# Performance work log

Measured on AMD Instinct MI355X. Metric: run time of the kernel, lower is better.

Reference implementation:

```python
import jax, jax.numpy as jnp
import numpy as np

MAX_RANGE = 100.0


def _conv3x3(x, w, b):
    # x: [B,C,H,W], w: [2,C,3,3], b: [2]
    y = jax.lax.conv_general_dilated(
        x, w, window_strides=(1, 1), padding='SAME',
        dimension_numbers=('NCHW', 'OIHW', 'NCHW'))
    return y + b[None, :, None, None]


def setup_inputs() -> dict:
    key = jax.random.key(0)
    k1, k2, k3 = jax.random.split(key, 3)
    B, C, H, W = 4, 64, 64, 64
    x = jax.random.normal(k1, (B, C, H, W), dtype=jnp.float32)
    conv_w = jax.random.normal(k2, (2, C, 3, 3), dtype=jnp.float32) * 0.05
    conv_b = jax.random.normal(k3, (2,), dtype=jnp.float32) * 0.05
    return {'x': x, 'conv_w': conv_w, 'conv_b': conv_b}


def reference(x, conv_w, conv_b):
    # alpha, beta: [B,1,H,W]
    ab = MAX_RANGE * jnp.tanh(_conv3x3(x, conv_w, conv_b))
    alpha, beta = ab[:, 0:1], ab[:, 1:2]

    # Pairwise differences d[b,i,j,h,w] = beta[b]*x[b,i] - x[b,j]  -> [B,C,C,H,W]
    d = beta[:, :, None] * x[:, :, None] - x[:, None, :]
    a = alpha[:, :, None]  # [B,1,1,H,W]

    # softAbs: softmax over the pair {d, -d} weighted by clamped alpha*d logits
    v1 = jnp.clip(d * a, -MAX_RANGE, MAX_RANGE)
    v2 = jnp.clip(-d * a, -MAX_RANGE, MAX_RANGE)
    m = jnp.maximum(v1, v2)
    e1 = jnp.exp(v1 - m)
    e2 = jnp.exp(v2 - m)
    p1 = e1 / (e1 + e2)
    sabs = d * (2.0 * p1 - 1.0)  # d*p1 + (-d)*(1-p1)

    # mean over i (the expand dim) -> [B,C,H,W]
    tmp = jnp.mean(sabs, axis=1)

    # softArgMin over channel dim
    sam = jax.nn.softmax(jnp.clip(-tmp * alpha, -MAX_RANGE, MAX_RANGE), axis=1)

    # soft median, keepdims -> [B,1,H,W]
    return jnp.sum(x * sam, axis=1, keepdims=True)
```

## Files before the change

kernel.cpp:

```cpp
#include <hip/hip_runtime.h>
#include <math.h>

#define MAXR 100.0f

__device__ __forceinline__ float tanh_fast(float s) {
    float as = fabsf(s);
    float e2 = __expf(-2.0f * as);
    float t  = (1.0f - e2) * __builtin_amdgcn_rcpf(1.0f + e2);
    return copysignf(t, s);
}

__global__ __launch_bounds__(256, 8) void dsf_fused(const float* __restrict__ x,
                                                    const float* __restrict__ wg,
                                                    const float* __restrict__ bias,
                                                    float* __restrict__ out) {
    __shared__ float xs[64 * 19];
    __shared__ float wl[1152];
    __shared__ float xst[4 * 68];

    const int tid  = threadIdx.x;
    const int lane = tid & 63;
    const int wave = tid >> 6;

    const int p0 = blockIdx.x * 4;
    const int b  = p0 >> 12;
    const int h  = (p0 >> 6) & 63;
    const int w0 = p0 & 63;

    for (int e = tid; e < 1152; e += 256) wl[e] = wg[e];

    const float* xbase = x + b * 262144;
    for (int e = tid; e < 1152; e += 256) {
        int c   = e / 18;
        int rem = e - c * 18;
        int r   = rem / 6;
        int wt  = rem - r * 6;
        int hh  = h + r - 1;
        int ww  = w0 - 1 + wt;
        float v = 0.f;
        if (hh >= 0 && hh < 64 && ww >= 0 && ww < 64)
            v = xbase[c * 4096 + hh * 64 + ww];
        xs[c * 19 + rem] = v;
        if (r == 1 && wt >= 1 && wt <= 4) xst[(wt - 1) * 68 + c] = v;
    }
    __syncthreads();

    const int p = p0 + wave;

    const float* xc  = xs + lane * 19;
    const float* wle = wl + lane * 9;
    float a0 = 0.f, a1 = 0.f;
    #pragma unroll
    for (int r = 0; r < 3; ++r) {
        #pragma unroll
        for (int t = 0; t < 3; ++t) {
            float xv = xc[r * 6 + wave + t];
            a0 = fmaf(xv, wle[r * 3 + t], a0);
            a1 = fmaf(xv, wle[576 + r * 3 + t], a1);
        }
    }
    #pragma unroll
    for (int off = 32; off; off >>= 1) {
        a0 += __shfl_xor(a0, off, 64);
        a1 += __shfl_xor(a1, off, 64);
    }
    const float al = MAXR * tanh_fast(a0 + bias[0]);
    const float be = MAXR * tanh_fast(a1 + bias[1]);
    const float aa = fabsf(al);
    const float n2aa = -2.0f * aa;

    const float* xr = xst + wave * 68;
    const float xj = xr[lane];
    float A = 0.0f;
    #pragma unroll 4
    for (int i = 0; i < 64; ++i) {
        float xi = xr[i];
        float dd = fmaf(be, xi, -xj);
        float ad = fabsf(dd);
        float e2 = __expf(n2aa * ad);
        float t  = (1.0f - e2) * __builtin_amdgcn_rcpf(1.0f + e2);
        A = fmaf(ad, t, A);
    }

    float gl = fmaxf(-A * aa * (1.0f / 64.0f), -MAXR);

    float gm = gl;
    #pragma unroll
    for (int off = 32; off; off >>= 1) gm = fmaxf(gm, __shfl_xor(gm, off, 64));
    float ew  = __expf(gl - gm);
    float den = ew, num = xj * ew;
    #pragma unroll
    for (int off = 32; off; off >>= 1) {
        den += __shfl_xor(den, off, 64);
        num += __shfl_xor(num, off, 64);
    }
    if (lane == 0) out[p] = num / den;
}

extern "C" void kernel_launch(void* const* d_in, const int* in_sizes, int n_in,
                              void* d_out, int out_size, void* d_ws, size_t ws_size,
                              hipStream_t stream) {
    const float* x      = (const float*)d_in[0];
    const float* conv_w = (const float*)d_in[1];
    const float* conv_b = (const float*)d_in[2];
    float* out = (float*)d_out;
    (void)d_ws; (void)ws_size;

    dsf_fused<<<4096, 256, 0, stream>>>(x, conv_w, conv_b, out);
}
```

Measured before the change: 85.64 us.

## Split into conv/transpose prep kernel and pairwise kernel using readlane broadcasts

Splits the fused kernel in two. A prep kernel, one block per image row, loads the row halo with float4 loads, computes the 3x3 conv for alpha and beta, and writes a channel-contiguous transpose of x to workspace. The pairwise kernel reads each pixel's 64 channels with a coalesced load and broadcasts x_i with readlane instead of LDS, using exp2/rcp intrinsics and four accumulators. This removes the redundant per-4-pixel halo loads and the scattered strided gathers, at the cost of a second launch and an extra workspace round-trip of x.

```diff
diff --git a/kernel.cpp b/kernel.cpp
--- a/kernel.cpp
+++ b/kernel.cpp
@@ -2,99 +2,147 @@
 #include <math.h>
 
 #define MAXR 100.0f
+#define LOG2E 1.4426950408889634f
+
+__device__ __forceinline__ float bcast_lane(float v, int i) {
+    return __int_as_float(__builtin_amdgcn_readlane(__float_as_int(v), i));
+}
+__device__ __forceinline__ float exp2_fast(float x) { return __builtin_amdgcn_exp2f(x); }
+__device__ __forceinline__ float rcp_fast(float x)  { return __builtin_amdgcn_rcpf(x); }
 
 __device__ __forceinline__ float tanh_fast(float s) {
-    float as = fabsf(s);
-    float e2 = __expf(-2.0f * as);
-    float t  = (1.0f - e2) * __builtin_amdgcn_rcpf(1.0f + e2);
+    float E = exp2_fast(2.0f * LOG2E * fabsf(s));
+    float t = fmaf(-2.0f, rcp_fast(E + 1.0f), 1.0f);
     return copysignf(t, s);
 }
 
-__global__ __launch_bounds__(256, 8) void dsf_fused(const float* __restrict__ x,
-                                                    const float* __restrict__ wg,
-                                                    const float* __restrict__ bias,
-                                                    float* __restrict__ out) {
-    __shared__ float xs[64 * 19];
+__global__ __launch_bounds__(256) void prep(const float* __restrict__ x,
+                                            const float* __restrict__ wg,
+                                            const float* __restrict__ bias,
+                                            float* __restrict__ xT,
+                                            float* __restrict__ alpha,
+                                            float* __restrict__ beta) {
+    __shared__ float xs[64 * 195];
     __shared__ float wl[1152];
-    __shared__ float xst[4 * 68];
 
-    const int tid  = threadIdx.x;
-    const int lane = tid & 63;
-    const int wave = tid >> 6;
-
-    const int p0 = blockIdx.x * 4;
-    const int b  = p0 >> 12;
-    const int h  = (p0 >> 6) & 63;
-    const int w0 = p0 & 63;
+    const int row = blockIdx.x;
+    const int b = row >> 6, h = row & 63;
+    const int tid = threadIdx.x, lane = tid & 63, g = tid >> 6;
+    const int l4 = lane & 15, quad = lane >> 4;
 
     for (int e = tid; e < 1152; e += 256) wl[e] = wg[e];
 
-    const float* xbase = x + b * 262144;
-    for (int e = tid; e < 1152; e += 256) {
-        int c   = e / 18;
-        int rem = e - c * 18;
-        int r   = rem / 6;
-        int wt  = rem - r * 6;
-        int hh  = h + r - 1;
-        int ww  = w0 - 1 + wt;
-        float v = 0.f;
-        if (hh >= 0 && hh < 64 && ww >= 0 && ww < 64)
-            v = xbase[c * 4096 + hh * 64 + ww];
-        xs[c * 19 + rem] = v;
-        if (r == 1 && wt >= 1 && wt <= 4) xst[(wt - 1) * 68 + c] = v;
+    const float* xb = x + b * 262144;
+    for (int pr = g * 4 + quad; pr < 192; pr += 16) {
+        int r = pr >> 6, c = pr & 63;
+        int hh = h + r - 1;
+        float4 v = make_float4(0.f, 0.f, 0.f, 0.f);
+        if (hh >= 0 && hh < 64)
+            v = *(const float4*)(xb + c * 4096 + hh * 64 + l4 * 4);
+        *(float4*)(xs + c * 195 + r * 65 + l4 * 4) = v;
     }
     __syncthreads();
 
-    const int p = p0 + wave;
+    float* xTrow = xT + row * 4096;
+    #pragma unroll
+    for (int wi = 0; wi < 16; ++wi) {
+        int wp = g * 16 + wi;
+        xTrow[wp * 64 + lane] = xs[lane * 195 + 65 + wp];
+    }
 
-    const float* xc  = xs + lane * 19;
-    const float* wle = wl + lane * 9;
-    float a0 = 0.f, a1 = 0.f;
+    float wr0[9], wr1[9];
     #pragma unroll
-    for (int r = 0; r < 3; ++r) {
+    for (int k = 0; k < 9; ++k) {
+        wr0[k] = wl[lane * 9 + k];
+        wr1[k] = wl[576 + lane * 9 + k];
+    }
+    const float b0 = bias[0], b1 = bias[1];
+    const float* xc = xs + lane * 195;
+
+    for (int wi = 0; wi < 16; ++wi) {
+        int wp = g * 16 + wi;
+        bool mL = (wp >= 1), mR = (wp <= 62);
+        float a0 = 0.f, a1 = 0.f;
         #pragma unroll
-        for (int t = 0; t < 3; ++t) {
-            float xv = xc[r * 6 + wave + t];
-            a0 = fmaf(xv, wle[r * 3 + t], a0);
-            a1 = fmaf(xv, wle[576 + r * 3 + t], a1);
+        for (int r = 0; r < 3; ++r) {
+            float xm = mL ? xc[r * 65 + wp - 1] : 0.f;
+            float x0 = xc[r * 65 + wp];
+            float xp = mR ? xc[r * 65 + wp + 1] : 0.f;
+            a0 = fmaf(xm, wr0[r * 3 + 0], a0);
+            a0 = fmaf(x0, wr0[r * 3 + 1], a0);
+            a0 = fmaf(xp, wr0[r * 3 + 2], a0);
+            a1 = fmaf(xm, wr1[r * 3 + 0], a1);
+            a1 = fmaf(x0, wr1[r * 3 + 1], a1);
+            a1 = fmaf(xp, wr1[r * 3 + 2], a1);
+        }
+        #pragma unroll
+        for (int off = 32; off; off >>= 1) {
+            a0 += __shfl_xor(a0, off, 64);
+            a1 += __shfl_xor(a1, off, 64);
+        }
+        if (lane == 0) {
+            alpha[row * 64 + wp] = MAXR * tanh_fast(a0 + b0);
+            beta [row * 64 + wp] = MAXR * tanh_fast(a1 + b1);
         }
     }
+}
+
+__global__ __launch_bounds__(256) void pairwise(const float* __restrict__ xT,
+                                                const float* __restrict__ alpha_g,
+                                                const float* __restrict__ beta_g,
+                                                float* __restrict__ out) {
+    const int tid = threadIdx.x, lane = tid & 63, wave = tid >> 6;
+    const int p = blockIdx.x * 4 + wave;
+
+    const float xj = xT[p * 64 + lane];
+    const float al = alpha_g[p];
+    const float be = beta_g[p];
+    const float aa = fabsf(al);
+    const float c2 = 2.0f * LOG2E * aa;
+
+    float A0 = 0.f, A1 = 0.f, A2 = 0.f, A3 = 0.f;
     #pragma unroll
-    for (int off = 32; off; off >>= 1) {
-        a0 += __shfl_xor(a0, off, 64);
-        a1 += __shfl_xor(a1, off, 64);
+    for (int i = 0; i < 64; i += 4) {
+        float s0 = bcast_lane(xj, i);
+        float s1 = bcast_lane(xj, i + 1);
+        float s2 = bcast_lane(xj, i + 2);
+        float s3 = bcast_lane(xj, i + 3);
+        float d0 = fmaf(be, s0, -xj);
+        float d1 = fmaf(be, s1, -xj);
+        float d2 = fmaf(be, s2, -xj);
+        float d3 = fmaf(be, s3, -xj);
+        float E0 = exp2_fast(c2 * fabsf(d0));
+        float E1 = exp2_fast(c2 * fabsf(d1));
+        float E2 = exp2_fast(c2 * fabsf(d2));
+        float E3 = exp2_fast(c2 * fabsf(d3));
+        float r0 = rcp_fast(E0 + 1.f);
+        float r1 = rcp_fast(E1 + 1.f);
+        float r2 = rcp_fast(E2 + 1.f);
+        float r3 = rcp_fast(E3 + 1.f);
+        float u0 = fmaf(-2.f, r0, 1.f);
+        float u1 = fmaf(-2.f, r1, 1.f);
+        float u2 = fmaf(-2.f, r2, 1.f);
+        float u3 = fmaf(-2.f, r3, 1.f);
+        A0 = fmaf(fabsf(d0), u0, A0);
+        A1 = fmaf(fabsf(d1), u1, A1);
+        A2 = fmaf(fabsf(d2), u2, A2);
+        A3 = fmaf(fabsf(d3), u3, A3);
     }
-    const float al = MAXR * tanh_fast(a0 + bias[0]);
-    const float be = MAXR * tanh_fast(a1 + bias[1]);
-    const float aa = fabsf(al);
-    const float n2aa = -2.0f * aa;
-
-    const float* xr = xst + wave * 68;
-    const float xj = xr[lane];
-    float A = 0.0f;
-    #pragma unroll 4
-    for (int i = 0; i < 64; ++i) {
-        float xi = xr[i];
-        float dd = fmaf(be, xi, -xj);
-        float ad = fabsf(dd);
-        float e2 = __expf(n2aa * ad);
-        float t  = (1.0f - e2) * __builtin_amdgcn_rcpf(1.0f + e2);
-        A = fmaf(ad, t, A);
-    }
+    float A = (A0 + A1) + (A2 + A3);
 
     float gl = fmaxf(-A * aa * (1.0f / 64.0f), -MAXR);
 
     float gm = gl;
     #pragma unroll
     for (int off = 32; off; off >>= 1) gm = fmaxf(gm, __shfl_xor(gm, off, 64));
-    float ew  = __expf(gl - gm);
+    float ew  = exp2_fast((gl - gm) * LOG2E);
     float den = ew, num = xj * ew;
     #pragma unroll
     for (int off = 32; off; off >>= 1) {
         den += __shfl_xor(den, off, 64);
         num += __shfl_xor(num, off, 64);
     }
-    if (lane == 0) out[p] = num / den;
+    if (lane == 0) out[p] = num * rcp_fast(den);
 }
 
 extern "C" void kernel_launch(void* const* d_in, const int* in_sizes, int n_in,
@@ -103,8 +151,12 @@
     const float* x      = (const float*)d_in[0];
     const float* conv_w = (const float*)d_in[1];
     const float* conv_b = (const float*)d_in[2];
-    float* out = (float*)d_out;
-    (void)d_ws; (void)ws_size;
+    float* out   = (float*)d_out;
 
-    dsf_fused<<<4096, 256, 0, stream>>>(x, conv_w, conv_b, out);
+    float* xT    = (float*)d_ws;
+    float* alpha = xT + 1048576;
+    float* beta  = alpha + 16384;
+
+    prep<<<256, 256, 0, stream>>>(x, conv_w, conv_b, xT, alpha, beta);
+    pairwise<<<4096, 256, 0, stream>>>(xT, alpha, beta, out);
 }
```

New measurement: 92.42 us. 7.9% more time.

## Keep conv weights in registers and broadcast channel values via readlane

Applied to the files above, without the earlier changes.

Each lane now loads its conv weights straight into registers, which removes the shared weight buffer and the transposed center-row buffer. The inner pairwise loop broadcasts x_i from lane registers with readlane instead of reading LDS. It is unrolled into four independent accumulators to expose more ILP. The tanh and exp paths now call the native exp2 and rcp builtins directly, and the launch-bounds occupancy hint is dropped, which may raise register use and lower occupancy.

```diff
diff --git a/kernel.cpp b/kernel.cpp
--- a/kernel.cpp
+++ b/kernel.cpp
@@ -2,21 +2,25 @@
 #include <math.h>
 
 #define MAXR 100.0f
+#define LOG2E 1.4426950408889634f
+
+__device__ __forceinline__ float bcast_lane(float v, int i) {
+    return __int_as_float(__builtin_amdgcn_readlane(__float_as_int(v), i));
+}
+__device__ __forceinline__ float exp2_fast(float x) { return __builtin_amdgcn_exp2f(x); }
+__device__ __forceinline__ float rcp_fast(float x)  { return __builtin_amdgcn_rcpf(x); }
 
 __device__ __forceinline__ float tanh_fast(float s) {
-    float as = fabsf(s);
-    float e2 = __expf(-2.0f * as);
-    float t  = (1.0f - e2) * __builtin_amdgcn_rcpf(1.0f + e2);
+    float E = exp2_fast(2.0f * LOG2E * fabsf(s));
+    float t = fmaf(-2.0f, rcp_fast(E + 1.0f), 1.0f);
     return copysignf(t, s);
 }
 
-__global__ __launch_bounds__(256, 8) void dsf_fused(const float* __restrict__ x,
-                                                    const float* __restrict__ wg,
-                                                    const float* __restrict__ bias,
-                                                    float* __restrict__ out) {
+__global__ __launch_bounds__(256) void dsf_fused(const float* __restrict__ x,
+                                                 const float* __restrict__ wg,
+                                                 const float* __restrict__ bias,
+                                                 float* __restrict__ out) {
     __shared__ float xs[64 * 19];
-    __shared__ float wl[1152];
-    __shared__ float xst[4 * 68];
 
     const int tid  = threadIdx.x;
     const int lane = tid & 63;
@@ -27,7 +31,13 @@
     const int h  = (p0 >> 6) & 63;
     const int w0 = p0 & 63;
 
-    for (int e = tid; e < 1152; e += 256) wl[e] = wg[e];
+    float wr0[9], wr1[9];
+    #pragma unroll
+    for (int k = 0; k < 9; ++k) {
+        wr0[k] = wg[lane * 9 + k];
+        wr1[k] = wg[576 + lane * 9 + k];
+    }
+    const float b0 = bias[0], b1 = bias[1];
 
     const float* xbase = x + b * 262144;
     for (int e = tid; e < 1152; e += 256) {
@@ -41,22 +51,18 @@
         if (hh >= 0 && hh < 64 && ww >= 0 && ww < 64)
             v = xbase[c * 4096 + hh * 64 + ww];
         xs[c * 19 + rem] = v;
-        if (r == 1 && wt >= 1 && wt <= 4) xst[(wt - 1) * 68 + c] = v;
     }
     __syncthreads();
 
-    const int p = p0 + wave;
-
-    const float* xc  = xs + lane * 19;
-    const float* wle = wl + lane * 9;
+    const float* xc = xs + lane * 19;
     float a0 = 0.f, a1 = 0.f;
     #pragma unroll
     for (int r = 0; r < 3; ++r) {
         #pragma unroll
         for (int t = 0; t < 3; ++t) {
             float xv = xc[r * 6 + wave + t];
-            a0 = fmaf(xv, wle[r * 3 + t], a0);
-            a1 = fmaf(xv, wle[576 + r * 3 + t], a1);
+            a0 = fmaf(xv, wr0[r * 3 + t], a0);
+            a1 = fmaf(xv, wr1[r * 3 + t], a1);
         }
     }
     #pragma unroll
@@ -64,37 +70,56 @@
         a0 += __shfl_xor(a0, off, 64);
         a1 += __shfl_xor(a1, off, 64);
     }
-    const float al = MAXR * tanh_fast(a0 + bias[0]);
-    const float be = MAXR * tanh_fast(a1 + bias[1]);
+    const float al = MAXR * tanh_fast(a0 + b0);
+    const float be = MAXR * tanh_fast(a1 + b1);
     const float aa = fabsf(al);
-    const float n2aa = -2.0f * aa;
+    const float c2 = 2.0f * LOG2E * aa;
 
-    const float* xr = xst + wave * 68;
-    const float xj = xr[lane];
-    float A = 0.0f;
-    #pragma unroll 4
-    for (int i = 0; i < 64; ++i) {
-        float xi = xr[i];
-        float dd = fmaf(be, xi, -xj);
-        float ad = fabsf(dd);
-        float e2 = __expf(n2aa * ad);
-        float t  = (1.0f - e2) * __builtin_amdgcn_rcpf(1.0f + e2);
-        A = fmaf(ad, t, A);
+    const float xj = xc[6 + wave + 1];
+
+    float A0 = 0.f, A1 = 0.f, A2 = 0.f, A3 = 0.f;
+    #pragma unroll
+    for (int i = 0; i < 16; ++i) {
+        float s0 = bcast_lane(xj, i);
+        float s1 = bcast_lane(xj, i + 16);
+        float s2 = bcast_lane(xj, i + 32);
+        float s3 = bcast_lane(xj, i + 48);
+        float d0 = fmaf(be, s0, -xj);
+        float d1 = fmaf(be, s1, -xj);
+        float d2 = fmaf(be, s2, -xj);
+        float d3 = fmaf(be, s3, -xj);
+        float E0 = exp2_fast(c2 * fabsf(d0));
+        float E1 = exp2_fast(c2 * fabsf(d1));
+        float E2 = exp2_fast(c2 * fabsf(d2));
+        float E3 = exp2_fast(c2 * fabsf(d3));
+        float r0 = rcp_fast(E0 + 1.f);
+        float r1 = rcp_fast(E1 + 1.f);
+        float r2 = rcp_fast(E2 + 1.f);
+        float r3 = rcp_fast(E3 + 1.f);
+        float u0 = fmaf(-2.f, r0, 1.f);
+        float u1 = fmaf(-2.f, r1, 1.f);
+        float u2 = fmaf(-2.f, r2, 1.f);
+        float u3 = fmaf(-2.f, r3, 1.f);
+        A0 = fmaf(fabsf(d0), u0, A0);
+        A1 = fmaf(fabsf(d1), u1, A1);
+        A2 = fmaf(fabsf(d2), u2, A2);
+        A3 = fmaf(fabsf(d3), u3, A3);
     }
+    float A = (A0 + A1) + (A2 + A3);
 
     float gl = fmaxf(-A * aa * (1.0f / 64.0f), -MAXR);
 
     float gm = gl;
     #pragma unroll
     for (int off = 32; off; off >>= 1) gm = fmaxf(gm, __shfl_xor(gm, off, 64));
-    float ew  = __expf(gl - gm);
+    float ew  = exp2_fast((gl - gm) * LOG2E);
     float den = ew, num = xj * ew;
     #pragma unroll
     for (int off = 32; off; off >>= 1) {
         den += __shfl_xor(den, off, 64);
         num += __shfl_xor(num, off, 64);
     }
-    if (lane == 0) out[p] = num / den;
+    if (lane == 0) out[p0 + wave] = num * rcp_fast(den);
 }
 
 extern "C" void kernel_launch(void* const* d_in, const int* in_sizes, int n_in,
```

Result: no change. 84.89 us (-0.9%).
